# Optimization experiments

Hardware: AMD Instinct MI355X
Metric: run time of the kernel (lower is better)

The kernel has to match this reference:

```python
import jax, jax.numpy as jnp
import numpy as np

N_EMBD = 1024
HEAD_SIZE = 64
WINDOW_SIZE = 256


def setup_inputs() -> dict:
    key = jax.random.key(0)
    kx, kk, kq, kv = jax.random.split(key, 4)
    B, T = 4, 4096
    x = jax.random.normal(kx, (B, T, N_EMBD), dtype=jnp.float32)
    # Linear(n_embd, head_size, bias=False): y = x @ W where W is [n_embd, head_size]
    scale = 1.0 / np.sqrt(N_EMBD)
    Wk = jax.random.normal(kk, (N_EMBD, HEAD_SIZE), dtype=jnp.float32) * scale
    Wq = jax.random.normal(kq, (N_EMBD, HEAD_SIZE), dtype=jnp.float32) * scale
    Wv = jax.random.normal(kv, (N_EMBD, HEAD_SIZE), dtype=jnp.float32) * scale
    return {"x": x, "Wk": Wk, "Wq": Wq, "Wv": Wv}


def reference(x, Wk, Wq, Wv):
    B, T, C = x.shape
    k = jnp.einsum('btc,ch->bth', x, Wk)  # [B,T,H]
    q = jnp.einsum('btc,ch->bth', x, Wq)
    v = jnp.einsum('btc,ch->bth', x, Wv)
    scale = k.shape[-1] ** -0.5
    weights = jnp.einsum('bqh,bkh->bqk', q, k) * scale  # [B,T,T]
    rows = jnp.arange(T)[:, None]
    cols = jnp.arange(T)[None, :]
    # causal AND within sliding window of WINDOW_SIZE
    mask = (rows >= cols) & (cols >= rows - WINDOW_SIZE + 1)
    weights = jnp.where(mask, weights, -jnp.inf)
    weights = jax.nn.softmax(weights, axis=-1)
    out = jnp.einsum('bqk,bkh->bqh', weights, v)  # [B,T,H]
    return out
```

## Files before the change

kernel.cpp:

```cpp
#include <hip/hip_runtime.h>
#include <float.h>

#define TSEQ 4096
#define CEMB 1024
#define NH 64
#define WIN 256

typedef __attribute__((ext_vector_type(8))) short  s16x8;
typedef __attribute__((ext_vector_type(4))) float  f32x4;
typedef unsigned short ush;

__device__ __forceinline__ void split2(float f, ush& hi, ush& lo) {
    unsigned b = __float_as_uint(f);
    hi = (ush)(b >> 16);
    float hf = __uint_as_float(b & 0xFFFF0000u);
    lo = (ush)(__float_as_uint(f - hf) >> 16);
}

__device__ __forceinline__ void split8(f32x4 a, f32x4 b, s16x8& hi, s16x8& lo) {
    #pragma unroll
    for (int j = 0; j < 4; ++j) { ush h, l; split2(a[j], h, l); hi[j] = (short)h; lo[j] = (short)l; }
    #pragma unroll
    for (int j = 0; j < 4; ++j) { ush h, l; split2(b[j], h, l); hi[4+j] = (short)h; lo[4+j] = (short)l; }
}

#define MFMA(a, b, c) __builtin_amdgcn_mfma_f32_16x16x32_bf16((a), (b), (c), 0, 0, 0)

__device__ __forceinline__ void load_lds16(const void* g, void* l) {
    __builtin_amdgcn_global_load_lds(
        (const __attribute__((address_space(1))) unsigned int*)g,
        (__attribute__((address_space(3))) unsigned int*)l, 16, 0, 0);
}

__global__ __launch_bounds__(256)
void w_convert(const float* __restrict__ Wk, const float* __restrict__ Wq,
               const float* __restrict__ Wv,
               ush* __restrict__ Wth, ush* __restrict__ Wtl)
{
    __shared__ ush Lh[64][66], Ll[64][66];
    const int m  = blockIdx.x >> 4;
    const int k0 = (blockIdx.x & 15) << 6;
    const float* src = (m == 0) ? Wk : ((m == 1) ? Wq : Wv);

    const int kr = threadIdx.x >> 2;
    const int cq = threadIdx.x & 3;
    #pragma unroll
    for (int j = 0; j < 4; ++j) {
        const f32x4 v = *(const f32x4*)&src[(k0 + kr) * NH + cq * 16 + j * 4];
        #pragma unroll
        for (int e = 0; e < 4; ++e) {
            ush h, l; split2(v[e], h, l);
            const int c = cq * 16 + j * 4 + e;
            Lh[c][kr] = h; Ll[c][kr] = l;
        }
    }
    __syncthreads();
    const int n  = threadIdx.x >> 2;
    const int kc = threadIdx.x & 3;
    const size_t ob = (size_t)(m * 64 + n) * CEMB + k0 + kc * 16;
    *(s16x8*)&Wth[ob]     = *(const s16x8*)&Lh[n][kc * 16];
    *(s16x8*)&Wth[ob + 8] = *(const s16x8*)&Lh[n][kc * 16 + 8];
    *(s16x8*)&Wtl[ob]     = *(const s16x8*)&Ll[n][kc * 16];
    *(s16x8*)&Wtl[ob + 8] = *(const s16x8*)&Ll[n][kc * 16 + 8];
}

__global__ __launch_bounds__(256)
void qkv_proj(const float* __restrict__ x,
              const ush* __restrict__ Wth, const ush* __restrict__ Wtl,
              ush* __restrict__ kbh, ush* __restrict__ kbl,
              ush* __restrict__ qbh, ush* __restrict__ qbl,
              ush* __restrict__ vbh, ush* __restrict__ vbl)
{
    __shared__ float Axs[2][32 * 64];
    __shared__ ush  Bh[192 * 64], Bl[192 * 64];

    const int tid = threadIdx.x;
    const int m0  = blockIdx.x << 5;
    const int w   = tid >> 6;
    const int ln  = tid & 63;
    const int l15 = tid & 15;
    const int g   = (tid >> 4) & 3;

    int dmr[2], dmc[2], dmbase[2];
    #pragma unroll
    for (int i = 0; i < 2; ++i) {
        const int d0 = w * 128 + i * 64;
        const int d  = d0 + ln;
        dmr[i] = d >> 4;
        dmc[i] = (d & 15) ^ (dmr[i] & 15);
        dmbase[i] = d0 * 4;
    }

    int bn[6], bc[6];
    #pragma unroll
    for (int i = 0; i < 6; ++i) {
        const int s = tid + (i << 8);
        bn[i] = s >> 3; bc[i] = s & 7;
    }

    f32x4 acc[2][3];
    #pragma unroll
    for (int i = 0; i < 2; ++i)
        #pragma unroll
        for (int j = 0; j < 3; ++j) acc[i][j] = (f32x4){0.f, 0.f, 0.f, 0.f};

    #pragma unroll
    for (int i = 0; i < 2; ++i)
        load_lds16(&x[(size_t)(m0 + dmr[i]) * CEMB + dmc[i] * 4], &Axs[0][dmbase[i]]);
    s16x8 wrh[6], wrl[6];
    #pragma unroll
    for (int i = 0; i < 6; ++i) {
        const size_t o = (size_t)bn[i] * CEMB + bc[i] * 8;
        wrh[i] = *(const s16x8*)&Wth[o];
        wrl[i] = *(const s16x8*)&Wtl[o];
    }

    for (int t = 0; t < 16; ++t) {
        const int cur = t & 1;
        #pragma unroll
        for (int i = 0; i < 6; ++i) {
            const int o = bn[i] * 64 + ((bc[i] ^ (bn[i] & 7)) << 3);
            *(s16x8*)&Bh[o] = wrh[i];
            *(s16x8*)&Bl[o] = wrl[i];
        }
        __syncthreads();

        if (t < 15) {
            #pragma unroll
            for (int i = 0; i < 2; ++i)
                load_lds16(&x[(size_t)(m0 + dmr[i]) * CEMB + (t + 1) * 64 + dmc[i] * 4],
                           &Axs[cur ^ 1][dmbase[i]]);
            #pragma unroll
            for (int i = 0; i < 6; ++i) {
                const size_t o = (size_t)bn[i] * CEMB + (t + 1) * 64 + bc[i] * 8;
                wrh[i] = *(const s16x8*)&Wth[o];
                wrl[i] = *(const s16x8*)&Wtl[o];
            }
        }

        #pragma unroll
        for (int ks = 0; ks < 2; ++ks) {
            s16x8 afh[2], afl[2], bfh[3], bfl[3];
            #pragma unroll
            for (int rt = 0; rt < 2; ++rt) {
                const int row = rt * 16 + l15;
                const int c0 = ks * 8 + g * 2;
                const f32x4 a0 = *(const f32x4*)&Axs[cur][row * 64 + ((c0     ^ l15) << 2)];
                const f32x4 a1 = *(const f32x4*)&Axs[cur][row * 64 + (((c0+1) ^ l15) << 2)];
                split8(a0, a1, afh[rt], afl[rt]);
            }
            #pragma unroll
            for (int ct = 0; ct < 3; ++ct) {
                const int n = w * 48 + ct * 16 + l15;
                const int o = n * 64 + (((ks * 4 + g) ^ (n & 7)) << 3);
                bfh[ct] = *(const s16x8*)&Bh[o];
                bfl[ct] = *(const s16x8*)&Bl[o];
            }
            __builtin_amdgcn_s_setprio(1);
            #pragma unroll
            for (int rt = 0; rt < 2; ++rt)
                #pragma unroll
                for (int ct = 0; ct < 3; ++ct) {
                    acc[rt][ct] = MFMA(afh[rt], bfh[ct], acc[rt][ct]);
                    acc[rt][ct] = MFMA(afh[rt], bfl[ct], acc[rt][ct]);
                    acc[rt][ct] = MFMA(afl[rt], bfh[ct], acc[rt][ct]);
                }
            __builtin_amdgcn_s_setprio(0);
        }
        __syncthreads();
    }

    #pragma unroll
    for (int ct = 0; ct < 3; ++ct) {
        const int colbase = w * 48 + ct * 16;
        ush *oph, *opl;
        if (colbase < 64)       { oph = kbh; opl = kbl; }
        else if (colbase < 128) { oph = qbh; opl = qbl; }
        else                    { oph = vbh; opl = vbl; }
        const int col = (colbase & 63) + l15;
        #pragma unroll
        for (int rt = 0; rt < 2; ++rt)
            #pragma unroll
            for (int r = 0; r < 4; ++r) {
                const size_t row = m0 + rt * 16 + g * 4 + r;
                ush h, l; split2(acc[rt][ct][r], h, l);
                oph[row * NH + col] = h;
                opl[row * NH + col] = l;
            }
    }
}

__global__ __launch_bounds__(256)
void v_transpose(const ush* __restrict__ vbh, const ush* __restrict__ vbl,
                 ush* __restrict__ vbTh, ush* __restrict__ vbTl)
{
    __shared__ ush Th[64][72], Tl[64][72];
    const int k0 = blockIdx.x << 6;
    const int b  = blockIdx.y;
    const int key = threadIdx.x >> 2;
    const int cp  = (threadIdx.x & 3) << 1;
    #pragma unroll
    for (int i = 0; i < 2; ++i) {
        const int c = cp + i;
        const size_t o = ((size_t)b * TSEQ + k0 + key) * NH + c * 8;
        const s16x8 h = *(const s16x8*)&vbh[o];
        const s16x8 l = *(const s16x8*)&vbl[o];
        #pragma unroll
        for (int j = 0; j < 8; ++j) {
            Th[c * 8 + j][key] = (ush)h[j];
            Tl[c * 8 + j][key] = (ush)l[j];
        }
    }
    __syncthreads();
    const int dim = threadIdx.x >> 2;
    const int kc  = threadIdx.x & 3;
    const size_t ob = ((size_t)b * 64 + dim) * TSEQ + k0 + kc * 16;
    *(s16x8*)&vbTh[ob]     = *(const s16x8*)&Th[dim][kc * 16];
    *(s16x8*)&vbTh[ob + 8] = *(const s16x8*)&Th[dim][kc * 16 + 8];
    *(s16x8*)&vbTl[ob]     = *(const s16x8*)&Tl[dim][kc * 16];
    *(s16x8*)&vbTl[ob + 8] = *(const s16x8*)&Tl[dim][kc * 16 + 8];
}

__global__ __launch_bounds__(256)
void attn_swin(const ush* __restrict__ qbh, const ush* __restrict__ qbl,
               const ush* __restrict__ kbh, const ush* __restrict__ kbl,
               const ush* __restrict__ vbTh, const ush* __restrict__ vbTl,
               float* __restrict__ out)
{
    __shared__ ush Kh[64 * 72], Kl[64 * 72];
    __shared__ ush Vth[64 * 72], Vtl[64 * 72];
    __shared__ ush Ph[4][16 * 64], Pl[4][16 * 64];

    const int tid = threadIdx.x;
    const int q0  = blockIdx.x << 6;
    const int b   = blockIdx.y;
    const size_t tb  = (size_t)b * TSEQ;
    const size_t vtb = (size_t)b * 64;
    const int w   = tid >> 6;
    const int l15 = tid & 15;
    const int g   = (tid >> 4) & 3;
    const int u   = l15 & 7;

    const int qrow = q0 + w * 16 + l15;

    s16x8 Qh[2], Ql[2];
    #pragma unroll
    for (int ks = 0; ks < 2; ++ks) {
        const size_t o = (tb + qrow) * NH + ks * 32 + g * 8;
        Qh[ks] = *(const s16x8*)&qbh[o];
        Ql[ks] = *(const s16x8*)&qbl[o];
    }

    f32x4 O[4];
    #pragma unroll
    for (int i = 0; i < 4; ++i) O[i] = (f32x4){0.f, 0.f, 0.f, 0.f};
    float m_run = -FLT_MAX, l_run = 0.f;

    int lo = q0 - (WIN - 1); if (lo < 0) lo = 0;
    const int t_lo = lo >> 6, t_hi = q0 >> 6;

    const int skey = tid >> 2;
    const int scp  = (tid & 3) << 1;

    for (int t = t_lo; t <= t_hi; ++t) {
        const int k0 = t << 6;
        __syncthreads();
        #pragma unroll
        for (int i = 0; i < 2; ++i) {
            const int c = scp + i;
            const size_t ko = (tb + k0 + skey) * NH + c * 8;
            const size_t vo = (vtb + skey) * TSEQ + k0 + c * 8;
            *(s16x8*)&Kh[skey * 72 + c * 8]  = *(const s16x8*)&kbh[ko];
            *(s16x8*)&Kl[skey * 72 + c * 8]  = *(const s16x8*)&kbl[ko];
            *(s16x8*)&Vth[skey * 72 + c * 8] = *(const s16x8*)&vbTh[vo];
            *(s16x8*)&Vtl[skey * 72 + c * 8] = *(const s16x8*)&vbTl[vo];
        }
        __syncthreads();

        f32x4 S[4];
        __builtin_amdgcn_s_setprio(1);
        #pragma unroll
        for (int kt = 0; kt < 4; ++kt) {
            f32x4 s = (f32x4){0.f, 0.f, 0.f, 0.f};
            #pragma unroll
            for (int ks = 0; ks < 2; ++ks) {
                const int o = (kt * 16 + l15) * 72 + ks * 32 + g * 8;
                const s16x8 kah = *(const s16x8*)&Kh[o];
                const s16x8 kal = *(const s16x8*)&Kl[o];
                s = MFMA(kah, Qh[ks], s);
                s = MFMA(kah, Ql[ks], s);
                s = MFMA(kal, Qh[ks], s);
            }
            S[kt] = s;
        }
        __builtin_amdgcn_s_setprio(0);

        float mt = -FLT_MAX;
        #pragma unroll
        for (int kt = 0; kt < 4; ++kt)
            #pragma unroll
            for (int r = 0; r < 4; ++r) {
                const int key = k0 + kt * 16 + g * 4 + r;
                const float s = S[kt][r] * 0.125f;
                S[kt][r] = s;
                if ((key <= qrow) && (key > qrow - WIN)) mt = fmaxf(mt, s);
            }
        mt = fmaxf(mt, __shfl_xor(mt, 16));
        mt = fmaxf(mt, __shfl_xor(mt, 32));
        const float mn  = fmaxf(m_run, mt);
        const float fsc = __expf(m_run - mn);

        float sum = 0.f;
        #pragma unroll
        for (int kt = 0; kt < 4; ++kt) {
            const int c2 = ((kt * 2 + (g >> 1)) + u) & 7;
            const int abase = l15 * 64 + c2 * 8 + (g & 1) * 4;
            #pragma unroll
            for (int rp = 0; rp < 4; rp += 2) {
                const int key0 = k0 + kt * 16 + g * 4 + rp;
                const bool v0 = (key0     <= qrow) && (key0     > qrow - WIN);
                const bool v1 = (key0 + 1 <= qrow) && (key0 + 1 > qrow - WIN);
                const float p0 = v0 ? __expf(S[kt][rp]     - mn) : 0.f;
                const float p1 = v1 ? __expf(S[kt][rp + 1] - mn) : 0.f;
                sum += p0 + p1;
                ush h0, lo0, h1, lo1;
                split2(p0, h0, lo0); split2(p1, h1, lo1);
                *(unsigned int*)&Ph[w][abase + rp] = (unsigned int)h0  | ((unsigned int)h1  << 16);
                *(unsigned int*)&Pl[w][abase + rp] = (unsigned int)lo0 | ((unsigned int)lo1 << 16);
            }
        }
        sum += __shfl_xor(sum, 16);
        sum += __shfl_xor(sum, 32);
        l_run = l_run * fsc + sum;
        m_run = mn;

        float fr[4];
        #pragma unroll
        for (int r = 0; r < 4; ++r) fr[r] = __shfl(fsc, g * 4 + r);
        #pragma unroll
        for (int dt = 0; dt < 4; ++dt)
            #pragma unroll
            for (int r = 0; r < 4; ++r) O[dt][r] *= fr[r];

        #pragma unroll
        for (int ks = 0; ks < 2; ++ks) {
            const int po = l15 * 64 + ((((ks * 4 + g)) + u) & 7) * 8;
            const s16x8 pah = *(const s16x8*)&Ph[w][po];
            const s16x8 pal = *(const s16x8*)&Pl[w][po];
            __builtin_amdgcn_s_setprio(1);
            #pragma unroll
            for (int dt = 0; dt < 4; ++dt) {
                const int vo = (dt * 16 + l15) * 72 + ks * 32 + g * 8;
                const s16x8 vbh8 = *(const s16x8*)&Vth[vo];
                const s16x8 vbl8 = *(const s16x8*)&Vtl[vo];
                O[dt] = MFMA(pah, vbh8, O[dt]);
                O[dt] = MFMA(pah, vbl8, O[dt]);
                O[dt] = MFMA(pal, vbh8, O[dt]);
            }
            __builtin_amdgcn_s_setprio(0);
        }
    }

    const float linv = 1.f / l_run;
    float fr[4];
    #pragma unroll
    for (int r = 0; r < 4; ++r) fr[r] = __shfl(linv, g * 4 + r);
    #pragma unroll
    for (int dt = 0; dt < 4; ++dt)
        #pragma unroll
        for (int r = 0; r < 4; ++r) {
            const int row = q0 + w * 16 + g * 4 + r;
            out[(tb + row) * NH + dt * 16 + l15] = O[dt][r] * fr[r];
        }
}

extern "C" void kernel_launch(void* const* d_in, const int* in_sizes, int n_in,
                              void* d_out, int out_size, void* d_ws, size_t ws_size,
                              hipStream_t stream)
{
    const float* x  = (const float*)d_in[0];
    const float* Wk = (const float*)d_in[1];
    const float* Wq = (const float*)d_in[2];
    const float* Wv = (const float*)d_in[3];
    float* out = (float*)d_out;

    const int Bn = in_sizes[0] / (TSEQ * CEMB);
    const size_t perBuf = (size_t)Bn * TSEQ * NH;

    ush* base = (ush*)d_ws;
    ush* kbh = base;
    ush* kbl = kbh + perBuf;
    ush* qbh = kbl + perBuf;
    ush* qbl = qbh + perBuf;
    ush* vbh = qbl + perBuf;
    ush* vbl = vbh + perBuf;
    ush* vbTh = vbl + perBuf;
    ush* vbTl = vbTh + perBuf;
    ush* Wth = vbTl + perBuf;
    ush* Wtl = Wth + 192 * CEMB;

    w_convert<<<dim3(48), dim3(256), 0, stream>>>(Wk, Wq, Wv, Wth, Wtl);
    qkv_proj<<<dim3((Bn * TSEQ) / 32), dim3(256), 0, stream>>>(x, Wth, Wtl,
                                                               kbh, kbl, qbh, qbl, vbh, vbl);
    v_transpose<<<dim3(TSEQ / 64, Bn), dim3(256), 0, stream>>>(vbh, vbl, vbTh, vbTl);
    attn_swin<<<dim3(TSEQ / 64, Bn), dim3(256), 0, stream>>>(qbh, qbl, kbh, kbl,
                                                             vbTh, vbTl, out);
}
```

Measured before the change: 143.8 us.

## Split attention key range across warps and pre-split x to bf16 in projection

In the attention kernel, each block now handles 32 queries instead of 64, and its four warps split the key tiles between two halves. K is read directly from global memory rather than staged through LDS, and V tiles are register-prefetched into double-buffered LDS. The two halves' partial softmax states are merged through shared memory at the end, which doubles the grid size and adds a merge step. In the QKV projection, x is loaded into registers two tiles ahead and split to hi/lo bf16 once when stored to LDS, replacing async global-to-LDS fp32 loads and the repeated per-fragment splitting.

Result: slower. 150.5 us (+4.7%).

```diff
diff --git a/kernel.cpp b/kernel.cpp
--- a/kernel.cpp
+++ b/kernel.cpp
@@ -25,12 +25,6 @@
 }
 
 #define MFMA(a, b, c) __builtin_amdgcn_mfma_f32_16x16x32_bf16((a), (b), (c), 0, 0, 0)
-
-__device__ __forceinline__ void load_lds16(const void* g, void* l) {
-    __builtin_amdgcn_global_load_lds(
-        (const __attribute__((address_space(1))) unsigned int*)g,
-        (__attribute__((address_space(3))) unsigned int*)l, 16, 0, 0);
-}
 
 __global__ __launch_bounds__(256)
 void w_convert(const float* __restrict__ Wk, const float* __restrict__ Wq,
@@ -71,31 +65,26 @@
               ush* __restrict__ qbh, ush* __restrict__ qbl,
               ush* __restrict__ vbh, ush* __restrict__ vbl)
 {
-    __shared__ float Axs[2][32 * 64];
-    __shared__ ush  Bh[192 * 64], Bl[192 * 64];
+    __shared__ ush Ah[2][32 * 64], Al[2][32 * 64];
+    __shared__ ush Bh[192 * 64], Bl[192 * 64];
 
     const int tid = threadIdx.x;
     const int m0  = blockIdx.x << 5;
     const int w   = tid >> 6;
-    const int ln  = tid & 63;
     const int l15 = tid & 15;
     const int g   = (tid >> 4) & 3;
 
-    int dmr[2], dmc[2], dmbase[2];
-    #pragma unroll
-    for (int i = 0; i < 2; ++i) {
-        const int d0 = w * 128 + i * 64;
-        const int d  = d0 + ln;
-        dmr[i] = d >> 4;
-        dmc[i] = (d & 15) ^ (dmr[i] & 15);
-        dmbase[i] = d0 * 4;
-    }
-
-    int bn[6], bc[6];
+    const int arow = tid >> 3;
+    const int ach  = tid & 7;
+    const float* xp = x + (size_t)(m0 + arow) * CEMB + ach * 8;
+    const int awo = arow * 64 + ((ach ^ (arow & 7)) << 3);
+
+    int bn[6], bc[6], bwo[6];
     #pragma unroll
     for (int i = 0; i < 6; ++i) {
         const int s = tid + (i << 8);
         bn[i] = s >> 3; bc[i] = s & 7;
+        bwo[i] = bn[i] * 64 + ((bc[i] ^ (bn[i] & 7)) << 3);
     }
 
     f32x4 acc[2][3];
@@ -104,10 +93,15 @@
         #pragma unroll
         for (int j = 0; j < 3; ++j) acc[i][j] = (f32x4){0.f, 0.f, 0.f, 0.f};
 
-    #pragma unroll
-    for (int i = 0; i < 2; ++i)
-        load_lds16(&x[(size_t)(m0 + dmr[i]) * CEMB + dmc[i] * 4], &Axs[0][dmbase[i]]);
+    f32x4 xA0, xA1, xB0, xB1;
     s16x8 wrh[6], wrl[6];
+
+    xA0 = *(const f32x4*)(xp);
+    xA1 = *(const f32x4*)(xp + 4);
+    { s16x8 vh, vl; split8(xA0, xA1, vh, vl);
+      *(s16x8*)&Ah[0][awo] = vh; *(s16x8*)&Al[0][awo] = vl; }
+    xB0 = *(const f32x4*)(xp + 64);
+    xB1 = *(const f32x4*)(xp + 68);
     #pragma unroll
     for (int i = 0; i < 6; ++i) {
         const size_t o = (size_t)bn[i] * CEMB + bc[i] * 8;
@@ -115,60 +109,66 @@
         wrl[i] = *(const s16x8*)&Wtl[o];
     }
 
-    for (int t = 0; t < 16; ++t) {
-        const int cur = t & 1;
-        #pragma unroll
-        for (int i = 0; i < 6; ++i) {
-            const int o = bn[i] * 64 + ((bc[i] ^ (bn[i] & 7)) << 3);
-            *(s16x8*)&Bh[o] = wrh[i];
-            *(s16x8*)&Bl[o] = wrl[i];
-        }
-        __syncthreads();
-
-        if (t < 15) {
-            #pragma unroll
-            for (int i = 0; i < 2; ++i)
-                load_lds16(&x[(size_t)(m0 + dmr[i]) * CEMB + (t + 1) * 64 + dmc[i] * 4],
-                           &Axs[cur ^ 1][dmbase[i]]);
-            #pragma unroll
-            for (int i = 0; i < 6; ++i) {
-                const size_t o = (size_t)bn[i] * CEMB + (t + 1) * 64 + bc[i] * 8;
-                wrh[i] = *(const s16x8*)&Wth[o];
-                wrl[i] = *(const s16x8*)&Wtl[o];
-            }
-        }
-
-        #pragma unroll
-        for (int ks = 0; ks < 2; ++ks) {
-            s16x8 afh[2], afl[2], bfh[3], bfl[3];
-            #pragma unroll
-            for (int rt = 0; rt < 2; ++rt) {
-                const int row = rt * 16 + l15;
-                const int c0 = ks * 8 + g * 2;
-                const f32x4 a0 = *(const f32x4*)&Axs[cur][row * 64 + ((c0     ^ l15) << 2)];
-                const f32x4 a1 = *(const f32x4*)&Axs[cur][row * 64 + (((c0+1) ^ l15) << 2)];
-                split8(a0, a1, afh[rt], afl[rt]);
-            }
-            #pragma unroll
-            for (int ct = 0; ct < 3; ++ct) {
-                const int n = w * 48 + ct * 16 + l15;
-                const int o = n * 64 + (((ks * 4 + g) ^ (n & 7)) << 3);
-                bfh[ct] = *(const s16x8*)&Bh[o];
-                bfl[ct] = *(const s16x8*)&Bl[o];
-            }
-            __builtin_amdgcn_s_setprio(1);
-            #pragma unroll
-            for (int rt = 0; rt < 2; ++rt)
-                #pragma unroll
-                for (int ct = 0; ct < 3; ++ct) {
-                    acc[rt][ct] = MFMA(afh[rt], bfh[ct], acc[rt][ct]);
-                    acc[rt][ct] = MFMA(afh[rt], bfl[ct], acc[rt][ct]);
-                    acc[rt][ct] = MFMA(afl[rt], bfh[ct], acc[rt][ct]);
-                }
-            __builtin_amdgcn_s_setprio(0);
-        }
-        __syncthreads();
-    }
+#define QKV_BODY(T, CUR, NXT, XW0, XW1, XL0, XL1)                                   \
+    {                                                                               \
+        _Pragma("unroll")                                                           \
+        for (int i = 0; i < 6; ++i) {                                               \
+            *(s16x8*)&Bh[bwo[i]] = wrh[i];                                          \
+            *(s16x8*)&Bl[bwo[i]] = wrl[i];                                          \
+        }                                                                           \
+        if ((T) < 15) {                                                             \
+            s16x8 vh, vl; split8(XW0, XW1, vh, vl);                                 \
+            *(s16x8*)&Ah[NXT][awo] = vh; *(s16x8*)&Al[NXT][awo] = vl;               \
+        }                                                                           \
+        __syncthreads();                                                            \
+        if ((T) < 14) {                                                             \
+            XL0 = *(const f32x4*)(xp + ((T) + 2) * 64);                             \
+            XL1 = *(const f32x4*)(xp + ((T) + 2) * 64 + 4);                         \
+        }                                                                           \
+        if ((T) < 15) {                                                             \
+            _Pragma("unroll")                                                       \
+            for (int i = 0; i < 6; ++i) {                                           \
+                const size_t o = (size_t)bn[i] * CEMB + ((T) + 1) * 64 + bc[i] * 8; \
+                wrh[i] = *(const s16x8*)&Wth[o];                                    \
+                wrl[i] = *(const s16x8*)&Wtl[o];                                    \
+            }                                                                       \
+        }                                                                           \
+        _Pragma("unroll")                                                           \
+        for (int ks = 0; ks < 2; ++ks) {                                            \
+            s16x8 afh[2], afl[2], bfh[3], bfl[3];                                   \
+            _Pragma("unroll")                                                       \
+            for (int rt = 0; rt < 2; ++rt) {                                        \
+                const int o = (rt * 16 + l15) * 64 + (((ks * 4 + g) ^ (l15 & 7)) << 3); \
+                afh[rt] = *(const s16x8*)&Ah[CUR][o];                               \
+                afl[rt] = *(const s16x8*)&Al[CUR][o];                               \
+            }                                                                       \
+            _Pragma("unroll")                                                       \
+            for (int ct = 0; ct < 3; ++ct) {                                        \
+                const int n = w * 48 + ct * 16 + l15;                               \
+                const int o = n * 64 + (((ks * 4 + g) ^ (n & 7)) << 3);             \
+                bfh[ct] = *(const s16x8*)&Bh[o];                                    \
+                bfl[ct] = *(const s16x8*)&Bl[o];                                    \
+            }                                                                       \
+            __builtin_amdgcn_s_setprio(1);                                          \
+            _Pragma("unroll")                                                       \
+            for (int rt = 0; rt < 2; ++rt)                                          \
+                _Pragma("unroll")                                                   \
+                for (int ct = 0; ct < 3; ++ct) {                                    \
+                    acc[rt][ct] = MFMA(afh[rt], bfh[ct], acc[rt][ct]);              \
+                    acc[rt][ct] = MFMA(afh[rt], bfl[ct], acc[rt][ct]);              \
+                    acc[rt][ct] = MFMA(afl[rt], bfh[ct], acc[rt][ct]);              \
+                }                                                                   \
+            __builtin_amdgcn_s_setprio(0);                                          \
+        }                                                                           \
+        __syncthreads();                                                            \
+    }
+
+    for (int tp = 0; tp < 8; ++tp) {
+        const int t0 = tp * 2;
+        QKV_BODY(t0,     0, 1, xB0, xB1, xA0, xA1)
+        QKV_BODY(t0 + 1, 1, 0, xA0, xA1, xB0, xB1)
+    }
+#undef QKV_BODY
 
     #pragma unroll
     for (int ct = 0; ct < 3; ++ct) {
@@ -227,21 +227,23 @@
                const ush* __restrict__ vbTh, const ush* __restrict__ vbTl,
                float* __restrict__ out)
 {
-    __shared__ ush Kh[64 * 72], Kl[64 * 72];
-    __shared__ ush Vth[64 * 72], Vtl[64 * 72];
+    __shared__ ush Vth[2][64 * 72], Vtl[2][64 * 72];
     __shared__ ush Ph[4][16 * 64], Pl[4][16 * 64];
+    __shared__ float cO[4][16][68];
+    __shared__ float cmx[4][16], cls[4][16];
 
     const int tid = threadIdx.x;
-    const int q0  = blockIdx.x << 6;
+    const int q0  = blockIdx.x << 5;
     const int b   = blockIdx.y;
-    const size_t tb  = (size_t)b * TSEQ;
-    const size_t vtb = (size_t)b * 64;
+    const size_t tb = (size_t)b * TSEQ;
     const int w   = tid >> 6;
     const int l15 = tid & 15;
     const int g   = (tid >> 4) & 3;
     const int u   = l15 & 7;
-
-    const int qrow = q0 + w * 16 + l15;
+    const int rg  = w & 1;
+    const int hf  = w >> 1;
+
+    const int qrow = q0 + rg * 16 + l15;
 
     s16x8 Qh[2], Ql[2];
     #pragma unroll
@@ -257,121 +259,169 @@
     float m_run = -FLT_MAX, l_run = 0.f;
 
     int lo = q0 - (WIN - 1); if (lo < 0) lo = 0;
-    const int t_lo = lo >> 6, t_hi = q0 >> 6;
-
-    const int skey = tid >> 2;
-    const int scp  = (tid & 3) << 1;
-
-    for (int t = t_lo; t <= t_hi; ++t) {
-        const int k0 = t << 6;
+    const int t_lo = lo >> 6, t_hi = (q0 + 31) >> 6;
+    const int nIter = (t_hi - t_lo + 2) >> 1;
+
+    const int sb = tid >> 7;
+    const int j  = tid & 127;
+    int sdim[4], sch[4];
+    #pragma unroll
+    for (int ii = 0; ii < 4; ++ii) {
+        const int it = j + (ii << 7);
+        sdim[ii] = it >> 3; sch[ii] = it & 7;
+    }
+    const size_t vrow = (size_t)b * 64;
+
+    s16x8 vrh[4], vrl[4];
+    int ts = t_lo + sb;
+    bool sv = ts <= t_hi;
+    if (sv) {
+        #pragma unroll
+        for (int ii = 0; ii < 4; ++ii) {
+            const size_t o = (vrow + sdim[ii]) * TSEQ + ts * 64 + sch[ii] * 8;
+            vrh[ii] = *(const s16x8*)&vbTh[o];
+            vrl[ii] = *(const s16x8*)&vbTl[o];
+        }
+    }
+
+    for (int i = 0; i < nIter; ++i) {
+        if (sv) {
+            #pragma unroll
+            for (int ii = 0; ii < 4; ++ii) {
+                const int lo_ = sdim[ii] * 72 + sch[ii] * 8;
+                *(s16x8*)&Vth[sb][lo_] = vrh[ii];
+                *(s16x8*)&Vtl[sb][lo_] = vrl[ii];
+            }
+        }
         __syncthreads();
-        #pragma unroll
-        for (int i = 0; i < 2; ++i) {
-            const int c = scp + i;
-            const size_t ko = (tb + k0 + skey) * NH + c * 8;
-            const size_t vo = (vtb + skey) * TSEQ + k0 + c * 8;
-            *(s16x8*)&Kh[skey * 72 + c * 8]  = *(const s16x8*)&kbh[ko];
-            *(s16x8*)&Kl[skey * 72 + c * 8]  = *(const s16x8*)&kbl[ko];
-            *(s16x8*)&Vth[skey * 72 + c * 8] = *(const s16x8*)&vbTh[vo];
-            *(s16x8*)&Vtl[skey * 72 + c * 8] = *(const s16x8*)&vbTl[vo];
+        const int tsn = t_lo + sb + 2 * (i + 1);
+        const bool svn = (i + 1 < nIter) && (tsn <= t_hi);
+        if (svn) {
+            #pragma unroll
+            for (int ii = 0; ii < 4; ++ii) {
+                const size_t o = (vrow + sdim[ii]) * TSEQ + tsn * 64 + sch[ii] * 8;
+                vrh[ii] = *(const s16x8*)&vbTh[o];
+                vrl[ii] = *(const s16x8*)&vbTl[o];
+            }
+        }
+
+        const int t = t_lo + hf + 2 * i;
+        if (t <= t_hi) {
+            const int k0 = t << 6;
+
+            f32x4 S[4];
+            __builtin_amdgcn_s_setprio(1);
+            #pragma unroll
+            for (int kt = 0; kt < 4; ++kt) {
+                f32x4 s = (f32x4){0.f, 0.f, 0.f, 0.f};
+                #pragma unroll
+                for (int ks = 0; ks < 2; ++ks) {
+                    const size_t o = (tb + k0 + kt * 16 + l15) * NH + ks * 32 + g * 8;
+                    const s16x8 kah = *(const s16x8*)&kbh[o];
+                    const s16x8 kal = *(const s16x8*)&kbl[o];
+                    s = MFMA(kah, Qh[ks], s);
+                    s = MFMA(kah, Ql[ks], s);
+                    s = MFMA(kal, Qh[ks], s);
+                }
+                S[kt] = s;
+            }
+            __builtin_amdgcn_s_setprio(0);
+
+            float mt = -FLT_MAX;
+            #pragma unroll
+            for (int kt = 0; kt < 4; ++kt)
+                #pragma unroll
+                for (int r = 0; r < 4; ++r) {
+                    const int key = k0 + kt * 16 + g * 4 + r;
+                    const float s = S[kt][r] * 0.125f;
+                    S[kt][r] = s;
+                    if ((key <= qrow) && (key > qrow - WIN)) mt = fmaxf(mt, s);
+                }
+            mt = fmaxf(mt, __shfl_xor(mt, 16));
+            mt = fmaxf(mt, __shfl_xor(mt, 32));
+            const float mn  = fmaxf(m_run, mt);
+            const float fsc = __expf(m_run - mn);
+
+            float sum = 0.f;
+            #pragma unroll
+            for (int kt = 0; kt < 4; ++kt) {
+                const int c2 = ((kt * 2 + (g >> 1)) + u) & 7;
+                const int abase = l15 * 64 + c2 * 8 + (g & 1) * 4;
+                #pragma unroll
+                for (int rp = 0; rp < 4; rp += 2) {
+                    const int key0 = k0 + kt * 16 + g * 4 + rp;
+                    const bool v0 = (key0     <= qrow) && (key0     > qrow - WIN);
+                    const bool v1 = (key0 + 1 <= qrow) && (key0 + 1 > qrow - WIN);
+                    const float p0 = v0 ? __expf(S[kt][rp]     - mn) : 0.f;
+                    const float p1 = v1 ? __expf(S[kt][rp + 1] - mn) : 0.f;
+                    sum += p0 + p1;
+                    ush h0, lo0, h1, lo1;
+                    split2(p0, h0, lo0); split2(p1, h1, lo1);
+                    *(unsigned int*)&Ph[w][abase + rp] = (unsigned int)h0  | ((unsigned int)h1  << 16);
+                    *(unsigned int*)&Pl[w][abase + rp] = (unsigned int)lo0 | ((unsigned int)lo1 << 16);
+                }
+            }
+            sum += __shfl_xor(sum, 16);
+            sum += __shfl_xor(sum, 32);
+            l_run = l_run * fsc + sum;
+            m_run = mn;
+
+            float fr[4];
+            #pragma unroll
+            for (int r = 0; r < 4; ++r) fr[r] = __shfl(fsc, g * 4 + r);
+            #pragma unroll
+            for (int dt = 0; dt < 4; ++dt)
+                #pragma unroll
+                for (int r = 0; r < 4; ++r) O[dt][r] *= fr[r];
+
+            #pragma unroll
+            for (int ks = 0; ks < 2; ++ks) {
+                const int po = l15 * 64 + (((ks * 4 + g) + u) & 7) * 8;
+                const s16x8 pah = *(const s16x8*)&Ph[w][po];
+                const s16x8 pal = *(const s16x8*)&Pl[w][po];
+                __builtin_amdgcn_s_setprio(1);
+                #pragma unroll
+                for (int dt = 0; dt < 4; ++dt) {
+                    const int vo = (dt * 16 + l15) * 72 + ks * 32 + g * 8;
+                    const s16x8 vh8 = *(const s16x8*)&Vth[hf][vo];
+                    const s16x8 vl8 = *(const s16x8*)&Vtl[hf][vo];
+                    O[dt] = MFMA(pah, vh8, O[dt]);
+                    O[dt] = MFMA(pah, vl8, O[dt]);
+                    O[dt] = MFMA(pal, vh8, O[dt]);
+                }
+                __builtin_amdgcn_s_setprio(0);
+            }
         }
         __syncthreads();
-
-        f32x4 S[4];
-        __builtin_amdgcn_s_setprio(1);
-        #pragma unroll
-        for (int kt = 0; kt < 4; ++kt) {
-            f32x4 s = (f32x4){0.f, 0.f, 0.f, 0.f};
-            #pragma unroll
-            for (int ks = 0; ks < 2; ++ks) {
-                const int o = (kt * 16 + l15) * 72 + ks * 32 + g * 8;
-                const s16x8 kah = *(const s16x8*)&Kh[o];
-                const s16x8 kal = *(const s16x8*)&Kl[o];
-                s = MFMA(kah, Qh[ks], s);
-                s = MFMA(kah, Ql[ks], s);
-                s = MFMA(kal, Qh[ks], s);
-            }
-            S[kt] = s;
-        }
-        __builtin_amdgcn_s_setprio(0);
-
-        float mt = -FLT_MAX;
-        #pragma unroll
-        for (int kt = 0; kt < 4; ++kt)
-            #pragma unroll
-            for (int r = 0; r < 4; ++r) {
-                const int key = k0 + kt * 16 + g * 4 + r;
-                const float s = S[kt][r] * 0.125f;
-                S[kt][r] = s;
-                if ((key <= qrow) && (key > qrow - WIN)) mt = fmaxf(mt, s);
-            }
-        mt = fmaxf(mt, __shfl_xor(mt, 16));
-        mt = fmaxf(mt, __shfl_xor(mt, 32));
-        const float mn  = fmaxf(m_run, mt);
-        const float fsc = __expf(m_run - mn);
-
-        float sum = 0.f;
-        #pragma unroll
-        for (int kt = 0; kt < 4; ++kt) {
-            const int c2 = ((kt * 2 + (g >> 1)) + u) & 7;
-            const int abase = l15 * 64 + c2 * 8 + (g & 1) * 4;
-            #pragma unroll
-            for (int rp = 0; rp < 4; rp += 2) {
-                const int key0 = k0 + kt * 16 + g * 4 + rp;
-                const bool v0 = (key0     <= qrow) && (key0     > qrow - WIN);
-                const bool v1 = (key0 + 1 <= qrow) && (key0 + 1 > qrow - WIN);
-                const float p0 = v0 ? __expf(S[kt][rp]     - mn) : 0.f;
-                const float p1 = v1 ? __expf(S[kt][rp + 1] - mn) : 0.f;
-                sum += p0 + p1;
-                ush h0, lo0, h1, lo1;
-                split2(p0, h0, lo0); split2(p1, h1, lo1);
-                *(unsigned int*)&Ph[w][abase + rp] = (unsigned int)h0  | ((unsigned int)h1  << 16);
-                *(unsigned int*)&Pl[w][abase + rp] = (unsigned int)lo0 | ((unsigned int)lo1 << 16);
-            }
-        }
-        sum += __shfl_xor(sum, 16);
-        sum += __shfl_xor(sum, 32);
-        l_run = l_run * fsc + sum;
-        m_run = mn;
-
-        float fr[4];
-        #pragma unroll
-        for (int r = 0; r < 4; ++r) fr[r] = __shfl(fsc, g * 4 + r);
-        #pragma unroll
-        for (int dt = 0; dt < 4; ++dt)
-            #pragma unroll
-            for (int r = 0; r < 4; ++r) O[dt][r] *= fr[r];
-
-        #pragma unroll
-        for (int ks = 0; ks < 2; ++ks) {
-            const int po = l15 * 64 + ((((ks * 4 + g)) + u) & 7) * 8;
-            const s16x8 pah = *(const s16x8*)&Ph[w][po];
-            const s16x8 pal = *(const s16x8*)&Pl[w][po];
-            __builtin_amdgcn_s_setprio(1);
-            #pragma unroll
-            for (int dt = 0; dt < 4; ++dt) {
-                const int vo = (dt * 16 + l15) * 72 + ks * 32 + g * 8;
-                const s16x8 vbh8 = *(const s16x8*)&Vth[vo];
-                const s16x8 vbl8 = *(const s16x8*)&Vtl[vo];
-                O[dt] = MFMA(pah, vbh8, O[dt]);
-                O[dt] = MFMA(pah, vbl8, O[dt]);
-                O[dt] = MFMA(pal, vbh8, O[dt]);
-            }
-            __builtin_amdgcn_s_setprio(0);
-        }
-    }
-
-    const float linv = 1.f / l_run;
-    float fr[4];
-    #pragma unroll
-    for (int r = 0; r < 4; ++r) fr[r] = __shfl(linv, g * 4 + r);
+        sv = svn; ts = tsn;
+    }
+
+    if (g == 0) { cmx[w][l15] = m_run; cls[w][l15] = l_run; }
     #pragma unroll
     for (int dt = 0; dt < 4; ++dt)
         #pragma unroll
-        for (int r = 0; r < 4; ++r) {
-            const int row = q0 + w * 16 + g * 4 + r;
-            out[(tb + row) * NH + dt * 16 + l15] = O[dt][r] * fr[r];
-        }
+        for (int r = 0; r < 4; ++r)
+            cO[w][g * 4 + r][dt * 16 + l15] = O[dt][r];
+    __syncthreads();
+
+    {
+        const int rg2 = w & 1, dh = w >> 1;
+        const float m0 = cmx[rg2][l15],     m1 = cmx[rg2 + 2][l15];
+        const float L0 = cls[rg2][l15],     L1 = cls[rg2 + 2][l15];
+        const float ms = fmaxf(m0, m1);
+        const float f0 = __expf(m0 - ms), f1 = __expf(m1 - ms);
+        const float rl = 1.0f / (f0 * L0 + f1 * L1);
+        #pragma unroll
+        for (int e2 = 0; e2 < 2; ++e2) {
+            f32x4 o;
+            #pragma unroll
+            for (int e = 0; e < 4; ++e) {
+                const int d = dh * 32 + g * 8 + e2 * 4 + e;
+                o[e] = (f0 * cO[rg2][l15][d] + f1 * cO[rg2 + 2][l15][d]) * rl;
+            }
+            *(f32x4*)&out[(tb + q0 + rg2 * 16 + l15) * NH + dh * 32 + g * 8 + e2 * 4] = o;
+        }
+    }
 }
 
 extern "C" void kernel_launch(void* const* d_in, const int* in_sizes, int n_in,
@@ -403,6 +453,6 @@
     qkv_proj<<<dim3((Bn * TSEQ) / 32), dim3(256), 0, stream>>>(x, Wth, Wtl,
                                                                kbh, kbl, qbh, qbl, vbh, vbl);
     v_transpose<<<dim3(TSEQ / 64, Bn), dim3(256), 0, stream>>>(vbh, vbl, vbTh, vbTl);
-    attn_swin<<<dim3(TSEQ / 64, Bn), dim3(256), 0, stream>>>(qbh, qbl, kbh, kbl,
+    attn_swin<<<dim3(TSEQ / 32, Bn), dim3(256), 0, stream>>>(qbh, qbl, kbh, kbl,
                                                              vbTh, vbTl, out);
 }
```
